# Optimization experiments

Hardware: AMD Instinct MI355X
Metric: run time of the kernel (lower is better)

The kernel has to match this reference:

```python
import jax, jax.numpy as jnp
import numpy as np

N_NODES = 50000
N_EDGES = 800000
IN_FEATS = 128
HID_FEATS = 256
OUT_FEATS = 256


def setup_inputs() -> dict:
    key = jax.random.key(0)
    ks = jax.random.split(key, 7)
    x = jax.random.normal(ks[0], (N_NODES, IN_FEATS), dtype=jnp.float32)
    src = jax.random.randint(ks[1], (N_EDGES,), 0, N_NODES, dtype=jnp.int64 if jax.config.jax_enable_x64 else jnp.int32)
    dst = jax.random.randint(ks[2], (N_EDGES,), 0, N_NODES, dtype=jnp.int64 if jax.config.jax_enable_x64 else jnp.int32)
    W1 = jax.random.normal(ks[3], (2 * IN_FEATS, HID_FEATS), dtype=jnp.float32) / np.sqrt(2 * IN_FEATS)
    b1 = jnp.zeros((HID_FEATS,), dtype=jnp.float32)
    W2 = jax.random.normal(ks[4], (2 * HID_FEATS, OUT_FEATS), dtype=jnp.float32) / np.sqrt(2 * HID_FEATS)
    b2 = jnp.zeros((OUT_FEATS,), dtype=jnp.float32)
    return {"x": x, "src": src, "dst": dst, "W1": W1, "b1": b1, "W2": W2, "b2": b2}


def reference(x, src, dst, W1, b1, W2, b2):
    n = x.shape[0]
    # in-degree per dst node (shared by both layers; zero-degree nodes get mean 0, matching DGL)
    deg = jax.ops.segment_sum(jnp.ones_like(dst, dtype=x.dtype), dst, num_segments=n)
    inv_deg = jnp.where(deg > 0, 1.0 / jnp.maximum(deg, 1.0), 0.0)[:, None]  # [N,1]

    def conv(h, W, b):
        # copy_u -> mean aggregation: gather src features [E,d], scatter-sum to dst, normalize
        h_neigh = jax.ops.segment_sum(h[src], dst, num_segments=n) * inv_deg  # [N,d]
        return jax.nn.relu(jnp.concatenate([h, h_neigh], axis=1) @ W + b)

    h = conv(x, W1, b1)   # [N, hid]
    return conv(h, W2, b2)  # [N, out]
```

## Files before the change

### kernel.cpp

```cpp
#include <hip/hip_runtime.h>
#include <hip/hip_bf16.h>
#include <cstdint>

constexpr int N_NODES = 50000;
constexpr int N_EDGES = 800000;
constexpr int F_IN    = 128;
constexpr int F_HID   = 256;
constexpr int N_COLS  = 256;
constexpr int M_PAD   = 50176;
constexpr int NB_F2BF = (N_NODES * F_IN / 4) / 256;

constexpr int EPB     = 4096;
constexpr int NB_PART = (N_EDGES + EPB - 1) / EPB;
constexpr int NBUCK   = (N_NODES + 255) / 256;

typedef unsigned short u16;
typedef u16   ushort4v __attribute__((ext_vector_type(4)));
typedef u16   ushort8v __attribute__((ext_vector_type(8)));
typedef __bf16 bf16x8  __attribute__((ext_vector_type(8)));
typedef float  f32x4   __attribute__((ext_vector_type(4)));

__device__ __forceinline__ float bf2f(u16 u) {
    return __uint_as_float(((uint32_t)u) << 16);
}
__device__ __forceinline__ u16 f2bf(float f) {
    uint32_t u = __float_as_uint(f);
    uint32_t r = u + 0x7FFFu + ((u >> 16) & 1u);
    return (u16)(r >> 16);
}

__device__ __forceinline__ void gll16(const void* g, void* l) {
    __builtin_amdgcn_global_load_lds(
        (const __attribute__((address_space(1))) uint32_t*)(uintptr_t)g,
        (__attribute__((address_space(3))) uint32_t*)(uintptr_t)l,
        16, 0, 0);
}

__global__ __launch_bounds__(256) void hist_kernel(const int* __restrict__ dst,
                                                   int* __restrict__ hist) {
    __shared__ int h[256];
    const int t = threadIdx.x;
    h[t] = 0;
    __syncthreads();
    const int base = blockIdx.x * EPB;
    #pragma unroll
    for (int i = 0; i < EPB / 256; ++i) {
        const int e = base + i * 256 + t;
        if (e < N_EDGES) atomicAdd(&h[dst[e] >> 8], 1);
    }
    __syncthreads();
    hist[blockIdx.x * 256 + t] = h[t];
}

__global__ __launch_bounds__(256) void colscan_kernel(int* __restrict__ hist,
                                                      int* __restrict__ bin_tot) {
    __shared__ int s[256];
    const int b = blockIdx.x;
    const int t = threadIdx.x;
    const int v = (t < NB_PART) ? hist[t * 256 + b] : 0;
    s[t] = v;
    __syncthreads();
    #pragma unroll
    for (int o = 1; o < 256; o <<= 1) {
        int tv = 0;
        if (t >= o) tv = s[t - o];
        __syncthreads();
        s[t] += tv;
        __syncthreads();
    }
    if (t < NB_PART) hist[t * 256 + b] = s[t] - v;
    if (t == 255) bin_tot[b] = s[255];
}

__global__ __launch_bounds__(256) void binscan_kernel(const int* __restrict__ bin_tot,
                                                      int* __restrict__ bin_base,
                                                      int* __restrict__ row_ptr) {
    __shared__ int s[256];
    const int t = threadIdx.x;
    const int v = (t < NBUCK) ? bin_tot[t] : 0;
    s[t] = v;
    __syncthreads();
    #pragma unroll
    for (int o = 1; o < 256; o <<= 1) {
        int tv = 0;
        if (t >= o) tv = s[t - o];
        __syncthreads();
        s[t] += tv;
        __syncthreads();
    }
    bin_base[t] = s[t] - v;
    if (t == 0) row_ptr[N_NODES] = N_EDGES;
}

__global__ __launch_bounds__(256) void scatter_kernel(const int* __restrict__ src,
                                                      const int* __restrict__ dst,
                                                      const int* __restrict__ hist,
                                                      const int* __restrict__ bin_base,
                                                      int2* __restrict__ ebuf) {
    __shared__ int cur[256];
    const int t = threadIdx.x;
    cur[t] = bin_base[t] + hist[blockIdx.x * 256 + t];
    __syncthreads();
    const int base = blockIdx.x * EPB;
    #pragma unroll
    for (int i = 0; i < EPB / 256; ++i) {
        const int e = base + i * 256 + t;
        if (e < N_EDGES) {
            const int d = dst[e];
            const int pos = atomicAdd(&cur[d >> 8], 1);
            ebuf[pos] = make_int2(src[e], d);
        }
    }
}

__global__ __launch_bounds__(256) void bucket_fill_kernel(const int2* __restrict__ ebuf,
                                                          const int* __restrict__ bin_base,
                                                          int* __restrict__ row_ptr,
                                                          float* __restrict__ inv_deg,
                                                          int* __restrict__ col) {
    __shared__ int cnt[256];
    __shared__ int scn[256];
    __shared__ int cur[256];
    const int blk = blockIdx.x;
    const int t = threadIdx.x;
    const int ebeg = bin_base[blk];
    const int eend = bin_base[blk + 1];
    const int nb0 = blk << 8;

    cnt[t] = 0;
    __syncthreads();
    for (int e = ebeg + t; e < eend; e += 256)
        atomicAdd(&cnt[ebuf[e].y & 255], 1);
    __syncthreads();
    const int d = cnt[t];
    scn[t] = d;
    __syncthreads();
    #pragma unroll
    for (int o = 1; o < 256; o <<= 1) {
        int tv = 0;
        if (t >= o) tv = scn[t - o];
        __syncthreads();
        scn[t] += tv;
        __syncthreads();
    }
    const int off = scn[t] - d;
    const int n = nb0 + t;
    if (n < N_NODES) {
        row_ptr[n] = ebeg + off;
        inv_deg[n] = (d > 0) ? (1.0f / (float)d) : 0.0f;
    }
    cur[t] = off;
    __syncthreads();
    for (int e = ebeg + t; e < eend; e += 256) {
        const int2 p = ebuf[e];
        col[ebeg + atomicAdd(&cur[p.y & 255], 1)] = p.x;
    }
}

__global__ __launch_bounds__(256) void prep_kernel(const float* __restrict__ x,
                                                   u16* __restrict__ xb,
                                                   const float* __restrict__ W1,
                                                   u16* __restrict__ W1t,
                                                   const float* __restrict__ W2,
                                                   u16* __restrict__ W2t) {
    const int b = blockIdx.x;
    const int tid = threadIdx.x;
    if (b < NB_F2BF) {
        const int i = b * 256 + tid;
        float4 v = *reinterpret_cast<const float4*>(&x[(size_t)i * 4]);
        ushort4v o;
        o.x = f2bf(v.x); o.y = f2bf(v.y); o.z = f2bf(v.z); o.w = f2bf(v.w);
        *reinterpret_cast<ushort4v*>(&xb[(size_t)i * 4]) = o;
    } else if (b < NB_F2BF + 256) {
        const int n = b - NB_F2BF;
        W1t[(size_t)n * 256 + tid] = f2bf(W1[(size_t)tid * N_COLS + n]);
    } else {
        const int n = b - (NB_F2BF + 256);
        #pragma unroll
        for (int kk = 0; kk < 2; ++kk) {
            const int k = kk * 256 + tid;
            W2t[(size_t)n * 512 + k] = f2bf(W2[(size_t)k * N_COLS + n]);
        }
    }
}

template <int F, int SLICES>
__global__ __launch_bounds__(256) void agg_mean_sliced(const u16* __restrict__ feat,
                                                       const int* __restrict__ rp,
                                                       const int* __restrict__ col,
                                                       const float* __restrict__ invd,
                                                       u16* __restrict__ out) {
    constexpr int SC  = F / SLICES;
    static_assert(SC == 64, "slice must be one 128B line");
    constexpr int LPN = SC / 8;
    constexpr int NPB = 256 / LPN;
    constexpr int XPS = 8 / SLICES;
    constexpr int NCHUNK = (N_NODES + NPB - 1) / NPB;
    constexpr int CPX    = (NCHUNK + XPS - 1) / XPS;
    const int bid  = blockIdx.x;
    const int x    = bid & 7;
    const int s    = x / XPS;
    const int part = x % XPS;
    const int chunk = part * CPX + (bid >> 3);
    const int slot = threadIdx.x / LPN;
    const int ln   = threadIdx.x % LPN;
    const int n = chunk * NPB + slot;
    if (n >= N_NODES) return;

    const u16* ft = feat + s * SC + ln * 8;
    const int beg = rp[n], end = rp[n + 1];
    float acc0[8] = {}, acc1[8] = {};
    int e = beg;
    for (; e + 3 < end; e += 4) {
        int nb0 = col[e];
        int nb1 = col[e + 1];
        int nb2 = col[e + 2];
        int nb3 = col[e + 3];
        ushort8v v0 = *reinterpret_cast<const ushort8v*>(&ft[(size_t)nb0 * F]);
        ushort8v v1 = *reinterpret_cast<const ushort8v*>(&ft[(size_t)nb1 * F]);
        ushort8v v2 = *reinterpret_cast<const ushort8v*>(&ft[(size_t)nb2 * F]);
        ushort8v v3 = *reinterpret_cast<const ushort8v*>(&ft[(size_t)nb3 * F]);
        #pragma unroll
        for (int j = 0; j < 8; ++j) acc0[j] += bf2f(v0[j]);
        #pragma unroll
        for (int j = 0; j < 8; ++j) acc1[j] += bf2f(v1[j]);
        #pragma unroll
        for (int j = 0; j < 8; ++j) acc0[j] += bf2f(v2[j]);
        #pragma unroll
        for (int j = 0; j < 8; ++j) acc1[j] += bf2f(v3[j]);
    }
    if (e + 1 < end) {
        int nb0 = col[e];
        int nb1 = col[e + 1];
        ushort8v v0 = *reinterpret_cast<const ushort8v*>(&ft[(size_t)nb0 * F]);
        ushort8v v1 = *reinterpret_cast<const ushort8v*>(&ft[(size_t)nb1 * F]);
        #pragma unroll
        for (int j = 0; j < 8; ++j) acc0[j] += bf2f(v0[j]);
        #pragma unroll
        for (int j = 0; j < 8; ++j) acc1[j] += bf2f(v1[j]);
        e += 2;
    }
    if (e < end) {
        ushort8v v = *reinterpret_cast<const ushort8v*>(&ft[(size_t)col[e] * F]);
        #pragma unroll
        for (int j = 0; j < 8; ++j) acc0[j] += bf2f(v[j]);
    }
    const float sc = invd[n];
    ushort8v o;
    #pragma unroll
    for (int j = 0; j < 8; ++j) o[j] = f2bf((acc0[j] + acc1[j]) * sc);
    *reinterpret_cast<ushort8v*>(&out[(size_t)n * F + s * SC + ln * 8]) = o;
}

template <int K1, bool OUT_BF16>
__global__ __launch_bounds__(256) void gemm_bt_bf16(const u16* __restrict__ A1,
                                                    const u16* __restrict__ A2,
                                                    const u16* __restrict__ Bt,
                                                    const float* __restrict__ bias,
                                                    void* __restrict__ Cout, int M) {
    constexpr int K = 2 * K1;
    __shared__ u16 As[128 * 64];
    __shared__ u16 Bs[128 * 64];

    const int t  = threadIdx.x;
    const int wv = t >> 6;
    const int l  = t & 63;
    const int g  = blockIdx.x >> 4;
    const int r  = blockIdx.x & 15;
    const int m0 = (g * 8 + (r & 7)) * 128;
    const int n0 = (r >> 3) * 128;

    const int srow = l >> 3;
    const int sjj  = ((l & 7) ^ srow) * 8;

    const int lr  = l & 15;
    const int l4  = l >> 4;
    const int wr  = (wv >> 1) * 64;
    const int wc  = (wv & 1) * 64;
    const int swz = lr & 7;

    f32x4 acc[4][4] = {};

    #pragma unroll 1
    for (int kt = 0; kt < K / 64; ++kt) {
        const int kg = kt * 64;
        const u16* Ab;
        int ka;
        if (kg < K1) { Ab = A1; ka = kg; }
        else         { Ab = A2; ka = kg - K1; }

        #pragma unroll
        for (int i = 0; i < 4; ++i) {
            const int rowg = wv * 32 + i * 8;
            gll16(&Ab[(size_t)(m0 + rowg + srow) * K1 + ka + sjj], &As[rowg * 64]);
            gll16(&Bt[(size_t)(n0 + rowg + srow) * K  + kg + sjj], &Bs[rowg * 64]);
        }
        __syncthreads();

        #pragma unroll
        for (int kk2 = 0; kk2 < 2; ++kk2) {
            const int jc = ((kk2 * 4 + l4) ^ swz) * 8;
            bf16x8 af[4], bfr[4];
            #pragma unroll
            for (int m = 0; m < 4; ++m)
                af[m] = *reinterpret_cast<const bf16x8*>(&As[(wr + m * 16 + lr) * 64 + jc]);
            #pragma unroll
            for (int n = 0; n < 4; ++n)
                bfr[n] = *reinterpret_cast<const bf16x8*>(&Bs[(wc + n * 16 + lr) * 64 + jc]);
            #pragma unroll
            for (int m = 0; m < 4; ++m)
                #pragma unroll
                for (int n = 0; n < 4; ++n)
                    acc[m][n] = __builtin_amdgcn_mfma_f32_16x16x32_bf16(af[m], bfr[n], acc[m][n], 0, 0, 0);
        }
        __syncthreads();
    }

    const int orow = (l >> 4) * 4;
    float bcol[4];
    #pragma unroll
    for (int n = 0; n < 4; ++n) bcol[n] = bias[n0 + wc + n * 16 + lr];

    #pragma unroll
    for (int m = 0; m < 4; ++m) {
        #pragma unroll
        for (int r2 = 0; r2 < 4; ++r2) {
            const int row = m0 + wr + m * 16 + orow + r2;
            if (row < M) {
                #pragma unroll
                for (int n = 0; n < 4; ++n) {
                    const int cg = n0 + wc + n * 16 + lr;
                    float v = fmaxf(acc[m][n][r2] + bcol[n], 0.f);
                    if (OUT_BF16)
                        ((u16*)Cout)[(size_t)row * N_COLS + cg] = f2bf(v);
                    else
                        ((float*)Cout)[(size_t)row * N_COLS + cg] = v;
                }
            }
        }
    }
}

extern "C" void kernel_launch(void* const* d_in, const int* in_sizes, int n_in,
                              void* d_out, int out_size, void* d_ws, size_t ws_size,
                              hipStream_t stream) {
    const float* x   = (const float*)d_in[0];
    const int*   src = (const int*)d_in[1];
    const int*   dst = (const int*)d_in[2];
    const float* W1  = (const float*)d_in[3];
    const float* b1  = (const float*)d_in[4];
    const float* W2  = (const float*)d_in[5];
    const float* b2  = (const float*)d_in[6];
    float* out = (float*)d_out;

    char* ws = (char*)d_ws;
    size_t off = 0;
    auto carve = [&](size_t bytes) {
        char* p = ws + off;
        off = (off + bytes + 255) & ~(size_t)255;
        return p;
    };
    int*   row_ptr  = (int*)carve(sizeof(int) * (N_NODES + 1));
    float* inv_deg  = (float*)carve(sizeof(float) * N_NODES);
    int*   col      = (int*)carve(sizeof(int) * N_EDGES);
    int*   hist     = (int*)carve(sizeof(int) * NB_PART * 256);
    int*   bin_tot  = (int*)carve(sizeof(int) * 256);
    int*   bin_base = (int*)carve(sizeof(int) * 256);
    int2*  ebuf     = (int2*)carve(sizeof(int2) * N_EDGES);
    u16*   xb       = (u16*)carve(sizeof(u16) * (size_t)M_PAD * F_IN);
    u16*   xnb      = (u16*)carve(sizeof(u16) * (size_t)M_PAD * F_IN);
    u16*   h1b      = (u16*)carve(sizeof(u16) * (size_t)M_PAD * F_HID);
    u16*   h1nb     = (u16*)carve(sizeof(u16) * (size_t)M_PAD * F_HID);
    u16*   W1t      = (u16*)carve(sizeof(u16) * 256 * 256);
    u16*   W2t      = (u16*)carve(sizeof(u16) * 256 * 512);

    hist_kernel<<<dim3(NB_PART), 256, 0, stream>>>(dst, hist);
    colscan_kernel<<<dim3(NBUCK), 256, 0, stream>>>(hist, bin_tot);
    binscan_kernel<<<dim3(1), 256, 0, stream>>>(bin_tot, bin_base, row_ptr);
    scatter_kernel<<<dim3(NB_PART), 256, 0, stream>>>(src, dst, hist, bin_base, ebuf);
    bucket_fill_kernel<<<dim3(NBUCK), 256, 0, stream>>>(ebuf, bin_base, row_ptr, inv_deg, col);

    prep_kernel<<<dim3(NB_F2BF + 512), 256, 0, stream>>>(x, xb, W1, W1t, W2, W2t);

    {
        constexpr int NPB = 32, XPS = 4;
        constexpr int CPX = (((N_NODES + NPB - 1) / NPB) + XPS - 1) / XPS;
        agg_mean_sliced<F_IN, 2><<<dim3(8 * CPX), 256, 0, stream>>>(
            xb, row_ptr, col, inv_deg, xnb);
    }
    gemm_bt_bf16<128, true><<<dim3(784), 256, 0, stream>>>(xb, xnb, W1t, b1, h1b, N_NODES);

    {
        constexpr int NPB = 32, XPS = 2;
        constexpr int CPX = (((N_NODES + NPB - 1) / NPB) + XPS - 1) / XPS;
        agg_mean_sliced<F_HID, 4><<<dim3(8 * CPX), 256, 0, stream>>>(
            h1b, row_ptr, col, inv_deg, h1nb);
    }
    gemm_bt_bf16<256, false><<<dim3(784), 256, 0, stream>>>(h1b, h1nb, W2t, b2, out, N_NODES);
}
```

Measured before the change: 164.7 us.

## Sort aggregation nodes by degree, pack edge buffer, fuse prep into histogram

Adds a degree histogram, scan and ordering pass so the mean-aggregation kernels handle nodes grouped by in-degree. This evens out per-warp loop trip counts and cuts divergence. The edge buffer is packed into one int (16-bit src, 8-bit local dst) to halve scatter traffic, and the cast/transpose prep kernel is merged into the histogram launch. The packing assumes node ids fit in 16 bits, but N_NODES is 50000, under 65536, so it holds. The degree order breaks node locality in the aggregation output writes and adds two small launches.

```diff
diff --git a/kernel.cpp b/kernel.cpp
--- a/kernel.cpp
+++ b/kernel.cpp
@@ -36,20 +36,45 @@
         16, 0, 0);
 }
 
-__global__ __launch_bounds__(256) void hist_kernel(const int* __restrict__ dst,
-                                                   int* __restrict__ hist) {
-    __shared__ int h[256];
-    const int t = threadIdx.x;
-    h[t] = 0;
-    __syncthreads();
-    const int base = blockIdx.x * EPB;
-    #pragma unroll
-    for (int i = 0; i < EPB / 256; ++i) {
-        const int e = base + i * 256 + t;
-        if (e < N_EDGES) atomicAdd(&h[dst[e] >> 8], 1);
-    }
-    __syncthreads();
-    hist[blockIdx.x * 256 + t] = h[t];
+__global__ __launch_bounds__(256) void hist_prep_kernel(const int* __restrict__ dst,
+                                                        int* __restrict__ hist,
+                                                        const float* __restrict__ x,
+                                                        u16* __restrict__ xb,
+                                                        const float* __restrict__ W1,
+                                                        u16* __restrict__ W1t,
+                                                        const float* __restrict__ W2,
+                                                        u16* __restrict__ W2t) {
+    const int b = blockIdx.x;
+    const int t = threadIdx.x;
+    if (b < NB_PART) {
+        __shared__ int h[256];
+        h[t] = 0;
+        __syncthreads();
+        const int base = b * EPB;
+        #pragma unroll
+        for (int i = 0; i < EPB / 256; ++i) {
+            const int e = base + i * 256 + t;
+            if (e < N_EDGES) atomicAdd(&h[dst[e] >> 8], 1);
+        }
+        __syncthreads();
+        hist[b * 256 + t] = h[t];
+    } else if (b < NB_PART + NB_F2BF) {
+        const int i = (b - NB_PART) * 256 + t;
+        float4 v = *reinterpret_cast<const float4*>(&x[(size_t)i * 4]);
+        ushort4v o;
+        o.x = f2bf(v.x); o.y = f2bf(v.y); o.z = f2bf(v.z); o.w = f2bf(v.w);
+        *reinterpret_cast<ushort4v*>(&xb[(size_t)i * 4]) = o;
+    } else if (b < NB_PART + NB_F2BF + 256) {
+        const int n = b - (NB_PART + NB_F2BF);
+        W1t[(size_t)n * 256 + t] = f2bf(W1[(size_t)t * N_COLS + n]);
+    } else {
+        const int n = b - (NB_PART + NB_F2BF + 256);
+        #pragma unroll
+        for (int kk = 0; kk < 2; ++kk) {
+            const int k = kk * 256 + t;
+            W2t[(size_t)n * 512 + k] = f2bf(W2[(size_t)k * N_COLS + n]);
+        }
+    }
 }
 
 __global__ __launch_bounds__(256) void colscan_kernel(int* __restrict__ hist,
@@ -74,7 +99,8 @@
 
 __global__ __launch_bounds__(256) void binscan_kernel(const int* __restrict__ bin_tot,
                                                       int* __restrict__ bin_base,
-                                                      int* __restrict__ row_ptr) {
+                                                      int* __restrict__ row_ptr,
+                                                      int* __restrict__ dhist) {
     __shared__ int s[256];
     const int t = threadIdx.x;
     const int v = (t < NBUCK) ? bin_tot[t] : 0;
@@ -89,6 +115,7 @@
         __syncthreads();
     }
     bin_base[t] = s[t] - v;
+    dhist[t] = 0;
     if (t == 0) row_ptr[N_NODES] = N_EDGES;
 }
 
@@ -96,7 +123,7 @@
                                                       const int* __restrict__ dst,
                                                       const int* __restrict__ hist,
                                                       const int* __restrict__ bin_base,
-                                                      int2* __restrict__ ebuf) {
+                                                      int* __restrict__ ebuf) {
     __shared__ int cur[256];
     const int t = threadIdx.x;
     cur[t] = bin_base[t] + hist[blockIdx.x * 256 + t];
@@ -108,16 +135,17 @@
         if (e < N_EDGES) {
             const int d = dst[e];
             const int pos = atomicAdd(&cur[d >> 8], 1);
-            ebuf[pos] = make_int2(src[e], d);
-        }
-    }
-}
-
-__global__ __launch_bounds__(256) void bucket_fill_kernel(const int2* __restrict__ ebuf,
+            ebuf[pos] = (src[e] & 0xFFFF) | ((d & 255) << 16);
+        }
+    }
+}
+
+__global__ __launch_bounds__(256) void bucket_fill_kernel(const int* __restrict__ ebuf,
                                                           const int* __restrict__ bin_base,
                                                           int* __restrict__ row_ptr,
                                                           float* __restrict__ inv_deg,
-                                                          int* __restrict__ col) {
+                                                          int* __restrict__ col,
+                                                          int* __restrict__ dhist) {
     __shared__ int cnt[256];
     __shared__ int scn[256];
     __shared__ int cur[256];
@@ -130,7 +158,7 @@
     cnt[t] = 0;
     __syncthreads();
     for (int e = ebeg + t; e < eend; e += 256)
-        atomicAdd(&cnt[ebuf[e].y & 255], 1);
+        atomicAdd(&cnt[(ebuf[e] >> 16) & 255], 1);
     __syncthreads();
     const int d = cnt[t];
     scn[t] = d;
@@ -148,39 +176,43 @@
     if (n < N_NODES) {
         row_ptr[n] = ebeg + off;
         inv_deg[n] = (d > 0) ? (1.0f / (float)d) : 0.0f;
+        atomicAdd(&dhist[d < 255 ? d : 255], 1);
     }
     cur[t] = off;
     __syncthreads();
     for (int e = ebeg + t; e < eend; e += 256) {
-        const int2 p = ebuf[e];
-        col[ebeg + atomicAdd(&cur[p.y & 255], 1)] = p.x;
-    }
-}
-
-__global__ __launch_bounds__(256) void prep_kernel(const float* __restrict__ x,
-                                                   u16* __restrict__ xb,
-                                                   const float* __restrict__ W1,
-                                                   u16* __restrict__ W1t,
-                                                   const float* __restrict__ W2,
-                                                   u16* __restrict__ W2t) {
-    const int b = blockIdx.x;
-    const int tid = threadIdx.x;
-    if (b < NB_F2BF) {
-        const int i = b * 256 + tid;
-        float4 v = *reinterpret_cast<const float4*>(&x[(size_t)i * 4]);
-        ushort4v o;
-        o.x = f2bf(v.x); o.y = f2bf(v.y); o.z = f2bf(v.z); o.w = f2bf(v.w);
-        *reinterpret_cast<ushort4v*>(&xb[(size_t)i * 4]) = o;
-    } else if (b < NB_F2BF + 256) {
-        const int n = b - NB_F2BF;
-        W1t[(size_t)n * 256 + tid] = f2bf(W1[(size_t)tid * N_COLS + n]);
-    } else {
-        const int n = b - (NB_F2BF + 256);
-        #pragma unroll
-        for (int kk = 0; kk < 2; ++kk) {
-            const int k = kk * 256 + tid;
-            W2t[(size_t)n * 512 + k] = f2bf(W2[(size_t)k * N_COLS + n]);
-        }
+        const int p = ebuf[e];
+        col[ebeg + atomicAdd(&cur[(p >> 16) & 255], 1)] = p & 0xFFFF;
+    }
+}
+
+__global__ __launch_bounds__(256) void dscan_kernel(const int* __restrict__ dhist,
+                                                    int* __restrict__ dcursor) {
+    __shared__ int s[256];
+    const int t = threadIdx.x;
+    const int v = dhist[t];
+    s[t] = v;
+    __syncthreads();
+    #pragma unroll
+    for (int o = 1; o < 256; o <<= 1) {
+        int tv = 0;
+        if (t >= o) tv = s[t - o];
+        __syncthreads();
+        s[t] += tv;
+        __syncthreads();
+    }
+    dcursor[t] = s[t] - v;
+}
+
+__global__ __launch_bounds__(256) void dorder_kernel(const int* __restrict__ rp,
+                                                     int* __restrict__ dcursor,
+                                                     int* __restrict__ order) {
+    const int n = blockIdx.x * 256 + threadIdx.x;
+    if (n < N_NODES) {
+        int d = rp[n + 1] - rp[n];
+        if (d > 255) d = 255;
+        const int pos = atomicAdd(&dcursor[d], 1);
+        order[pos] = n;
     }
 }
 
@@ -189,6 +221,7 @@
                                                        const int* __restrict__ rp,
                                                        const int* __restrict__ col,
                                                        const float* __restrict__ invd,
+                                                       const int* __restrict__ order,
                                                        u16* __restrict__ out) {
     constexpr int SC  = F / SLICES;
     static_assert(SC == 64, "slice must be one 128B line");
@@ -204,8 +237,9 @@
     const int chunk = part * CPX + (bid >> 3);
     const int slot = threadIdx.x / LPN;
     const int ln   = threadIdx.x % LPN;
-    const int n = chunk * NPB + slot;
-    if (n >= N_NODES) return;
+    const int gs = chunk * NPB + slot;
+    if (gs >= N_NODES) return;
+    const int n = order[gs];
 
     const u16* ft = feat + s * SC + ln * 8;
     const int beg = rp[n], end = rp[n + 1];
@@ -366,7 +400,10 @@
     int*   hist     = (int*)carve(sizeof(int) * NB_PART * 256);
     int*   bin_tot  = (int*)carve(sizeof(int) * 256);
     int*   bin_base = (int*)carve(sizeof(int) * 256);
-    int2*  ebuf     = (int2*)carve(sizeof(int2) * N_EDGES);
+    int*   dhist    = (int*)carve(sizeof(int) * 256);
+    int*   dcursor  = (int*)carve(sizeof(int) * 256);
+    int*   order    = (int*)carve(sizeof(int) * N_NODES);
+    int*   ebuf     = (int*)carve(sizeof(int) * N_EDGES);
     u16*   xb       = (u16*)carve(sizeof(u16) * (size_t)M_PAD * F_IN);
     u16*   xnb      = (u16*)carve(sizeof(u16) * (size_t)M_PAD * F_IN);
     u16*   h1b      = (u16*)carve(sizeof(u16) * (size_t)M_PAD * F_HID);
@@ -374,19 +411,21 @@
     u16*   W1t      = (u16*)carve(sizeof(u16) * 256 * 256);
     u16*   W2t      = (u16*)carve(sizeof(u16) * 256 * 512);
 
-    hist_kernel<<<dim3(NB_PART), 256, 0, stream>>>(dst, hist);
+    hist_prep_kernel<<<dim3(NB_PART + NB_F2BF + 512), 256, 0, stream>>>(
+        dst, hist, x, xb, W1, W1t, W2, W2t);
     colscan_kernel<<<dim3(NBUCK), 256, 0, stream>>>(hist, bin_tot);
-    binscan_kernel<<<dim3(1), 256, 0, stream>>>(bin_tot, bin_base, row_ptr);
+    binscan_kernel<<<dim3(1), 256, 0, stream>>>(bin_tot, bin_base, row_ptr, dhist);
     scatter_kernel<<<dim3(NB_PART), 256, 0, stream>>>(src, dst, hist, bin_base, ebuf);
-    bucket_fill_kernel<<<dim3(NBUCK), 256, 0, stream>>>(ebuf, bin_base, row_ptr, inv_deg, col);
-
-    prep_kernel<<<dim3(NB_F2BF + 512), 256, 0, stream>>>(x, xb, W1, W1t, W2, W2t);
+    bucket_fill_kernel<<<dim3(NBUCK), 256, 0, stream>>>(ebuf, bin_base, row_ptr, inv_deg, col, dhist);
+
+    dscan_kernel<<<dim3(1), 256, 0, stream>>>(dhist, dcursor);
+    dorder_kernel<<<dim3(NBUCK), 256, 0, stream>>>(row_ptr, dcursor, order);
 
     {
         constexpr int NPB = 32, XPS = 4;
         constexpr int CPX = (((N_NODES + NPB - 1) / NPB) + XPS - 1) / XPS;
         agg_mean_sliced<F_IN, 2><<<dim3(8 * CPX), 256, 0, stream>>>(
-            xb, row_ptr, col, inv_deg, xnb);
+            xb, row_ptr, col, inv_deg, order, xnb);
     }
     gemm_bt_bf16<128, true><<<dim3(784), 256, 0, stream>>>(xb, xnb, W1t, b1, h1b, N_NODES);
 
@@ -394,7 +433,7 @@
         constexpr int NPB = 32, XPS = 2;
         constexpr int CPX = (((N_NODES + NPB - 1) / NPB) + XPS - 1) / XPS;
         agg_mean_sliced<F_HID, 4><<<dim3(8 * CPX), 256, 0, stream>>>(
-            h1b, row_ptr, col, inv_deg, h1nb);
+            h1b, row_ptr, col, inv_deg, order, h1nb);
     }
     gemm_bt_bf16<256, false><<<dim3(784), 256, 0, stream>>>(h1b, h1nb, W2t, b2, out, N_NODES);
 }
```

New measurement: 438.2 us. 166% more time.
